# Kernel optimization log

Hardware: AMD Instinct MI355X
Metric: run time of the kernel (lower is better)

## Reference

```python
import jax, jax.numpy as jnp
import numpy as np

N_NODES = 100000
N_EDGES = 1600000
DIM = 128


def setup_inputs() -> dict:
    key = jax.random.key(0)
    k1, k2, k3, k4 = jax.random.split(key, 4)
    x = jax.random.normal(k1, (N_NODES, DIM), dtype=jnp.float32)
    edge_index = jax.random.randint(k2, (2, N_EDGES), 0, N_NODES, dtype=jnp.int64)
    scale = 1.0 / np.sqrt(DIM)
    W1 = jax.random.normal(k3, (DIM, DIM), dtype=jnp.float32) * scale
    W2 = jax.random.normal(k4, (DIM, DIM), dtype=jnp.float32) * scale
    b1 = jnp.zeros((DIM,), dtype=jnp.float32)
    b2 = jnp.zeros((DIM,), dtype=jnp.float32)
    return {"x": x, "edge_index": edge_index, "W1": W1, "b1": b1, "W2": W2, "b2": b2}


def _gcn_conv(x, src, dst, dinv, W, b, n):
    # linear transform first (PyG GCNConv), then normalized scatter-add aggregation
    h = x @ W                                   # [N, out]
    norm = dinv[src] * dinv[dst]                # [E+N]
    msg = h[src] * norm[:, None]                # [E+N, out]
    agg = jax.ops.segment_sum(msg, dst, num_segments=n)
    return agg + b


def reference(x, edge_index, W1, b1, W2, b2):
    n = x.shape[0]
    loops = jnp.arange(n, dtype=edge_index.dtype)
    src = jnp.concatenate([edge_index[0], loops])  # add self-loops
    dst = jnp.concatenate([edge_index[1], loops])
    deg = jax.ops.segment_sum(jnp.ones_like(src, dtype=x.dtype), dst, num_segments=n)
    dinv = jnp.where(deg > 0, jax.lax.rsqrt(deg), 0.0)  # D^{-1/2}
    h = _gcn_conv(x, src, dst, dinv, W1, b1, n)
    h = jax.nn.relu(h)
    out = _gcn_conv(h, src, dst, dinv, W2, b2, n)
    return out
```

## Files before the change

### kernel.cpp

```cpp
#include <hip/hip_runtime.h>
#include <hip/hip_bf16.h>
#include <hip/hip_fp16.h>

#define NN 100000
#define DIM 128
#define NB 391
#define BCAP 5120
#define GTILES ((NN + 63) / 64)
#define STP 130

typedef _Float16 f16x8 __attribute__((ext_vector_type(8)));
typedef float f32x4 __attribute__((ext_vector_type(4)));

__global__ void k_zero(int* __restrict__ p, int n) {
    int i = blockIdx.x * blockDim.x + threadIdx.x;
    if (i < n) p[i] = 0;
}

__global__ void k_binA(const int* __restrict__ src, const int* __restrict__ dst,
                       int* __restrict__ bcur, int* __restrict__ binbuf, int E) {
    __shared__ int hist[4][NB];
    const int t  = threadIdx.x;
    const int wv = t >> 6;
    for (int i = t; i < 4 * NB; i += 256) ((int*)hist)[i] = 0;
    __syncthreads();

    const int e0 = blockIdx.x * 4096;
    int mys[16], myd[16];
#pragma unroll
    for (int i = 0; i < 16; ++i) {
        const int e = e0 + i * 256 + t;
        int d = -1, s = 0;
        if (e < E) {
            d = dst[e];
            s = src[e];
            atomicAdd(&hist[wv][d >> 8], 1);
        }
        mys[i] = s;
        myd[i] = d;
    }
    __syncthreads();

    for (int b = t; b < NB; b += 256) {
        const int h0 = hist[0][b], h1 = hist[1][b], h2 = hist[2][b], h3 = hist[3][b];
        const int tot = h0 + h1 + h2 + h3;
        const int base = tot ? atomicAdd(&bcur[b], tot) : 0;
        hist[0][b] = base;
        hist[1][b] = base + h0;
        hist[2][b] = base + h0 + h1;
        hist[3][b] = base + h0 + h1 + h2;
    }
    __syncthreads();

#pragma unroll
    for (int i = 0; i < 16; ++i) {
        const int d = myd[i];
        if (d >= 0) {
            const int b = d >> 8;
            const int p = atomicAdd(&hist[wv][b], 1);
            if (p < BCAP) binbuf[b * BCAP + p] = mys[i] | ((d & 255) << 17);
        }
    }
}

__global__ void k_binCount(const int* __restrict__ bcur, const int* __restrict__ binbuf,
                           int* __restrict__ degi, float* __restrict__ dinv,
                           int* __restrict__ bsum) {
    __shared__ int cnt[4][256];
    __shared__ int red[256];
    const int b  = blockIdx.x;
    const int t  = threadIdx.x;
    const int wv = t >> 6;
#pragma unroll
    for (int w = 0; w < 4; ++w) cnt[w][t] = 0;
    __syncthreads();
    const int n = min(bcur[b], BCAP);
    const int* p = &binbuf[b * BCAP];
    for (int i = t; i < n; i += 256) atomicAdd(&cnt[wv][p[i] >> 17], 1);
    __syncthreads();
    const int node = b * 256 + t;
    const int c = cnt[0][t] + cnt[1][t] + cnt[2][t] + cnt[3][t];
    if (node < NN) {
        degi[node] = c;
        dinv[node] = rsqrtf((float)(c + 1));
    }
    red[t] = (node < NN) ? c : 0;
    __syncthreads();
    for (int d = 128; d > 0; d >>= 1) {
        if (t < d) red[t] += red[t + d];
        __syncthreads();
    }
    if (t == 0) bsum[b] = red[0];
}

__global__ void k_scan2(int* __restrict__ bsum, int nb) {
    __shared__ int s[1024];
    const int t = threadIdx.x;
    const int v = (t < nb) ? bsum[t] : 0;
    s[t] = v;
    __syncthreads();
    int acc = v;
    for (int d = 1; d < 1024; d <<= 1) {
        const int o = (t >= d) ? s[t - d] : 0;
        __syncthreads();
        acc += o;
        s[t] = acc;
        __syncthreads();
    }
    if (t < nb) bsum[t] = acc - v;
}

__global__ void k_gemm1(const float* __restrict__ inF, const float* __restrict__ W,
                        const float* __restrict__ dinv, _Float16* __restrict__ outH,
                        const int* __restrict__ degi, const int* __restrict__ bsum,
                        int* __restrict__ rowptr, const int* __restrict__ bcur,
                        const int* __restrict__ binbuf, int* __restrict__ csr) {
    __shared__ int s[256];
    __shared__ int cur[256];
    __shared__ _Float16 st[64][STP];
    const int t = threadIdx.x;

    if (blockIdx.x < NB) {
        const int b = blockIdx.x;
        const int node = b * 256 + t;
        const int deg = (node < NN) ? degi[node] : 0;
        s[t] = deg;
        __syncthreads();
        int acc = deg;
        for (int d = 1; d < 256; d <<= 1) {
            const int o = (t >= d) ? s[t - d] : 0;
            __syncthreads();
            acc += o;
            s[t] = acc;
            __syncthreads();
        }
        const int ex = acc - deg + bsum[b];
        cur[t] = ex;
        if (node < NN) {
            rowptr[node] = ex;
            if (node == NN - 1) rowptr[NN] = ex + deg;
        }
        __syncthreads();
        const int n = min(bcur[b], BCAP);
        const int* p = &binbuf[b * BCAP];
        for (int i = t; i < n; i += 256) {
            const int v = p[i];
            const int pos = atomicAdd(&cur[v >> 17], 1);
            csr[pos] = v & 0x1FFFF;
        }
        return;
    }

    const int tile = blockIdx.x - NB;
    const int row0 = tile * 64;
    const int wv   = t >> 6;
    const int l    = t & 63;
    const int l15  = l & 15;
    const int lk8  = (l >> 4) << 3;
    const int colw = wv << 5;

    f16x8 bf[2][4];
#pragma unroll
    for (int ct = 0; ct < 2; ++ct)
#pragma unroll
        for (int kt = 0; kt < 4; ++kt) {
            const int nn = colw + ct * 16 + l15;
            const int k0 = kt * 32 + lk8;
            f16x8 v;
#pragma unroll
            for (int j = 0; j < 8; ++j) v[j] = (_Float16)W[(k0 + j) * DIM + nn];
            bf[ct][kt] = v;
        }

    f32x4 acc[4][2];
#pragma unroll
    for (int rt = 0; rt < 4; ++rt)
#pragma unroll
        for (int ct = 0; ct < 2; ++ct) acc[rt][ct] = (f32x4){0.f, 0.f, 0.f, 0.f};

#pragma unroll
    for (int rt = 0; rt < 4; ++rt) {
        int row = row0 + rt * 16 + l15;
        row = min(row, NN - 1);
        f16x8 a[4];
#pragma unroll
        for (int kt = 0; kt < 4; ++kt) {
            const int k0 = kt * 32 + lk8;
            const float4 v0 = *(const float4*)&inF[row * DIM + k0];
            const float4 v1 = *(const float4*)&inF[row * DIM + k0 + 4];
            f16x8 v;
            v[0] = (_Float16)v0.x; v[1] = (_Float16)v0.y;
            v[2] = (_Float16)v0.z; v[3] = (_Float16)v0.w;
            v[4] = (_Float16)v1.x; v[5] = (_Float16)v1.y;
            v[6] = (_Float16)v1.z; v[7] = (_Float16)v1.w;
            a[kt] = v;
        }
#pragma unroll
        for (int ct = 0; ct < 2; ++ct)
#pragma unroll
            for (int kt = 0; kt < 4; ++kt)
                acc[rt][ct] = __builtin_amdgcn_mfma_f32_16x16x32_f16(a[kt], bf[ct][kt],
                                                                    acc[rt][ct], 0, 0, 0);
    }

#pragma unroll
    for (int rt = 0; rt < 4; ++rt)
#pragma unroll
        for (int r = 0; r < 4; ++r) {
            const int lr = rt * 16 + ((l >> 4) << 2) + r;
            const float d = dinv[min(row0 + lr, NN - 1)];
            st[lr][colw + l15]      = (_Float16)(acc[rt][0][r] * d);
            st[lr][colw + 16 + l15] = (_Float16)(acc[rt][1][r] * d);
        }
    __syncthreads();
#pragma unroll
    for (int i = 0; i < 4; ++i) {
        const int lr  = (wv << 4) + (i << 2) + (l >> 4);
        const int row = row0 + lr;
        if (row < NN) {
            const uint4 v = *(const uint4*)&st[lr][l15 << 3];
            *(uint4*)&outH[row * DIM + (l15 << 3)] = v;
        }
    }
}

__global__ void k_gemm2(const _Float16* __restrict__ inH, const float* __restrict__ W,
                        const float* __restrict__ dinv, _Float16* __restrict__ outH) {
    __shared__ _Float16 st[64][STP];
    const int t = threadIdx.x;
    const int row0 = blockIdx.x * 64;
    const int wv   = t >> 6;
    const int l    = t & 63;
    const int l15  = l & 15;
    const int lk8  = (l >> 4) << 3;
    const int colw = wv << 5;

    f16x8 bf[2][4];
#pragma unroll
    for (int ct = 0; ct < 2; ++ct)
#pragma unroll
        for (int kt = 0; kt < 4; ++kt) {
            const int nn = colw + ct * 16 + l15;
            const int k0 = kt * 32 + lk8;
            f16x8 v;
#pragma unroll
            for (int j = 0; j < 8; ++j) v[j] = (_Float16)W[(k0 + j) * DIM + nn];
            bf[ct][kt] = v;
        }

    f32x4 acc[4][2];
#pragma unroll
    for (int rt = 0; rt < 4; ++rt)
#pragma unroll
        for (int ct = 0; ct < 2; ++ct) acc[rt][ct] = (f32x4){0.f, 0.f, 0.f, 0.f};

#pragma unroll
    for (int rt = 0; rt < 4; ++rt) {
        int row = row0 + rt * 16 + l15;
        row = min(row, NN - 1);
        f16x8 a[4];
#pragma unroll
        for (int kt = 0; kt < 4; ++kt)
            a[kt] = *(const f16x8*)&inH[row * DIM + kt * 32 + lk8];
#pragma unroll
        for (int ct = 0; ct < 2; ++ct)
#pragma unroll
            for (int kt = 0; kt < 4; ++kt)
                acc[rt][ct] = __builtin_amdgcn_mfma_f32_16x16x32_f16(a[kt], bf[ct][kt],
                                                                    acc[rt][ct], 0, 0, 0);
    }

#pragma unroll
    for (int rt = 0; rt < 4; ++rt)
#pragma unroll
        for (int r = 0; r < 4; ++r) {
            const int lr = rt * 16 + ((l >> 4) << 2) + r;
            const float d = dinv[min(row0 + lr, NN - 1)];
            st[lr][colw + l15]      = (_Float16)(acc[rt][0][r] * d);
            st[lr][colw + 16 + l15] = (_Float16)(acc[rt][1][r] * d);
        }
    __syncthreads();
#pragma unroll
    for (int i = 0; i < 4; ++i) {
        const int lr  = (wv << 4) + (i << 2) + (l >> 4);
        const int row = row0 + lr;
        if (row < NN) {
            const uint4 v = *(const uint4*)&st[lr][l15 << 3];
            *(uint4*)&outH[row * DIM + (l15 << 3)] = v;
        }
    }
}

template <int FINAL>
__global__ void k_gather(const _Float16* __restrict__ hsp, _Float16* __restrict__ aggH,
                         float* __restrict__ outF, const int* __restrict__ csr,
                         const int* __restrict__ rowptr, const float* __restrict__ dinv,
                         const float* __restrict__ bias) {
    const __half* __restrict__ hs = (const __half*)hsp;
    const int w = (blockIdx.x * blockDim.x + threadIdx.x) >> 6;
    if (w >= NN) return;
    const int lane = threadIdx.x & 63;
    const int off  = lane << 1;

    const int start = __builtin_amdgcn_readfirstlane(rowptr[w]);
    const int end   = __builtin_amdgcn_readfirstlane(rowptr[w + 1]);

    float2 a0 = __half22float2(*(const __half2*)&hs[w * DIM + off]);
    float2 a1 = {0.f, 0.f}, a2 = {0.f, 0.f}, a3 = {0.f, 0.f};

    int j = start;
    for (; j + 3 < end; j += 4) {
        const int s0 = __builtin_amdgcn_readfirstlane(csr[j]);
        const int s1 = __builtin_amdgcn_readfirstlane(csr[j + 1]);
        const int s2 = __builtin_amdgcn_readfirstlane(csr[j + 2]);
        const int s3 = __builtin_amdgcn_readfirstlane(csr[j + 3]);
        const float2 v0 = __half22float2(*(const __half2*)&hs[s0 * DIM + off]);
        const float2 v1 = __half22float2(*(const __half2*)&hs[s1 * DIM + off]);
        const float2 v2 = __half22float2(*(const __half2*)&hs[s2 * DIM + off]);
        const float2 v3 = __half22float2(*(const __half2*)&hs[s3 * DIM + off]);
        a0.x += v0.x; a0.y += v0.y;
        a1.x += v1.x; a1.y += v1.y;
        a2.x += v2.x; a2.y += v2.y;
        a3.x += v3.x; a3.y += v3.y;
    }
    for (; j < end; ++j) {
        const int s0 = __builtin_amdgcn_readfirstlane(csr[j]);
        const float2 v0 = __half22float2(*(const __half2*)&hs[s0 * DIM + off]);
        a0.x += v0.x; a0.y += v0.y;
    }

    const float d = dinv[w];
    const float2 bb = {bias[off], bias[off + 1]};
    float2 r = {a0.x + a1.x + a2.x + a3.x, a0.y + a1.y + a2.y + a3.y};
    if constexpr (FINAL) {
        float2 o;
        o.x = fmaf(d, r.x, bb.x);
        o.y = fmaf(d, r.y, bb.y);
        *(float2*)&outF[w * DIM + off] = o;
    } else {
        r.x = fmaxf(fmaf(d, r.x, bb.x), 0.f);
        r.y = fmaxf(fmaf(d, r.y, bb.y), 0.f);
        *(__half2*)&aggH[w * DIM + off] = __floats2half2_rn(r.x, r.y);
    }
}

extern "C" void kernel_launch(void* const* d_in, const int* in_sizes, int n_in,
                              void* d_out, int out_size, void* d_ws, size_t ws_size,
                              hipStream_t stream) {
    const float* x  = (const float*)d_in[0];
    const int*   ei = (const int*)d_in[1];
    const float* W1 = (const float*)d_in[2];
    const float* b1 = (const float*)d_in[3];
    const float* W2 = (const float*)d_in[4];
    const float* b2 = (const float*)d_in[5];
    float* out = (float*)d_out;

    const int E = in_sizes[1] / 2;
    const int* src = ei;
    const int* dst = ei + E;

    char* ws = (char*)d_ws;
    float*    dinv   = (float*)(ws);
    int*      degi   = (int*)  (ws + (1  << 20));
    int*      rowptr = (int*)  (ws + (2  << 20));
    int*      bsum   = (int*)  (ws + (3  << 20));
    int*      bcur   = (int*)  (ws + (3  << 20) + 65536);
    int*      csr    = (int*)  (ws + (4  << 20));
    int*      binbuf = (int*)  (ws + (11 << 20));
    _Float16* hs     = (_Float16*)(ws + (20 << 20));
    _Float16* aggH   = (_Float16*)(ws + (47 << 20));
    _Float16* hs2    = (_Float16*)(ws + (74 << 20));

    const int ABLK = (E + 4095) / 4096;

    k_zero    <<<(NB + 255) / 256, 256, 0, stream>>>(bcur, NB);
    k_binA    <<<ABLK, 256, 0, stream>>>(src, dst, bcur, binbuf, E);
    k_binCount<<<NB, 256, 0, stream>>>(bcur, binbuf, degi, dinv, bsum);
    k_scan2   <<<1, 1024, 0, stream>>>(bsum, NB);

    k_gemm1<<<NB + GTILES, 256, 0, stream>>>(x, W1, dinv, hs, degi, bsum,
                                             rowptr, bcur, binbuf, csr);
    k_gather<0><<<(NN * 64) / 256, 256, 0, stream>>>(hs, aggH, nullptr, csr, rowptr,
                                                     dinv, b1);

    k_gemm2<<<GTILES, 256, 0, stream>>>(aggH, W2, dinv, hs2);
    k_gather<1><<<(NN * 64) / 256, 256, 0, stream>>>(hs2, nullptr, out, csr, rowptr,
                                                     dinv, b2);
}
```

Before: 225.7 us.

## Fold degree counting into CSR build, pre-transpose weights, move dinv scaling into gather

Removes the separate bin-count kernel. The block scan now runs directly on per-bin edge counts, and degree counting, dinv and rowptr are computed inside the CSR-building blocks of gemm1. Because dinv is no longer available when the GEMM tiles run, layer-1 source-side dinv scaling moves into gather1, which loads dinv per neighbour. W1 and W2 are pre-transposed to fp16 once so GEMM blocks can load B fragments as vectors, and the gather loops are unrolled to 8. The per-edge dinv loads in gather1 add extra scattered memory traffic in exchange for the removed launch and the overlap of CSR building with the GEMM.

```diff
diff --git a/kernel.cpp b/kernel.cpp
--- a/kernel.cpp
+++ b/kernel.cpp
@@ -12,9 +12,22 @@
 typedef _Float16 f16x8 __attribute__((ext_vector_type(8)));
 typedef float f32x4 __attribute__((ext_vector_type(4)));
 
-__global__ void k_zero(int* __restrict__ p, int n) {
-    int i = blockIdx.x * blockDim.x + threadIdx.x;
-    if (i < n) p[i] = 0;
+__global__ void k_init(const float* __restrict__ W1, const float* __restrict__ W2,
+                       int* __restrict__ bcur, _Float16* __restrict__ Wt1,
+                       _Float16* __restrict__ Wt2) {
+    const int b = blockIdx.x;
+    const int t = threadIdx.x;
+    if (b < 2) {
+        const int i = b * 256 + t;
+        if (i < NB) bcur[i] = 0;
+        return;
+    }
+    const int idx = (b - 2) * 256 + t;
+    const int which = idx >> 14;
+    const int i = idx & 16383;
+    const int n = i >> 7, k = i & 127;
+    if (which == 0) Wt1[n * DIM + k] = (_Float16)W1[k * DIM + n];
+    else            Wt2[n * DIM + k] = (_Float16)W2[k * DIM + n];
 }
 
 __global__ void k_binA(const int* __restrict__ src, const int* __restrict__ dst,
@@ -63,89 +76,70 @@
     }
 }
 
-__global__ void k_binCount(const int* __restrict__ bcur, const int* __restrict__ binbuf,
-                           int* __restrict__ degi, float* __restrict__ dinv,
-                           int* __restrict__ bsum) {
-    __shared__ int cnt[4][256];
-    __shared__ int red[256];
-    const int b  = blockIdx.x;
+__global__ void k_scan2(const int* __restrict__ bcur, int* __restrict__ bbase, int nb) {
+    __shared__ int s[512];
+    const int t = threadIdx.x;
+    const int v = (t < nb) ? bcur[t] : 0;
+    s[t] = v;
+    __syncthreads();
+    int acc = v;
+    for (int d = 1; d < 512; d <<= 1) {
+        const int o = (t >= d) ? s[t - d] : 0;
+        __syncthreads();
+        acc += o;
+        s[t] = acc;
+        __syncthreads();
+    }
+    if (t < nb) bbase[t] = acc - v;
+}
+
+__global__ void k_gemm1(const float* __restrict__ inF, const _Float16* __restrict__ Wt,
+                        _Float16* __restrict__ outH, const int* __restrict__ bbase,
+                        const int* __restrict__ bcur, const int* __restrict__ binbuf,
+                        int* __restrict__ rowptr, float* __restrict__ dinv,
+                        int* __restrict__ csr) {
+    __shared__ int cnt4[4][256];
+    __shared__ int sc[256];
+    __shared__ _Float16 st[64][STP];
     const int t  = threadIdx.x;
     const int wv = t >> 6;
-#pragma unroll
-    for (int w = 0; w < 4; ++w) cnt[w][t] = 0;
-    __syncthreads();
-    const int n = min(bcur[b], BCAP);
-    const int* p = &binbuf[b * BCAP];
-    for (int i = t; i < n; i += 256) atomicAdd(&cnt[wv][p[i] >> 17], 1);
-    __syncthreads();
-    const int node = b * 256 + t;
-    const int c = cnt[0][t] + cnt[1][t] + cnt[2][t] + cnt[3][t];
-    if (node < NN) {
-        degi[node] = c;
-        dinv[node] = rsqrtf((float)(c + 1));
-    }
-    red[t] = (node < NN) ? c : 0;
-    __syncthreads();
-    for (int d = 128; d > 0; d >>= 1) {
-        if (t < d) red[t] += red[t + d];
-        __syncthreads();
-    }
-    if (t == 0) bsum[b] = red[0];
-}
-
-__global__ void k_scan2(int* __restrict__ bsum, int nb) {
-    __shared__ int s[1024];
-    const int t = threadIdx.x;
-    const int v = (t < nb) ? bsum[t] : 0;
-    s[t] = v;
-    __syncthreads();
-    int acc = v;
-    for (int d = 1; d < 1024; d <<= 1) {
-        const int o = (t >= d) ? s[t - d] : 0;
-        __syncthreads();
-        acc += o;
-        s[t] = acc;
-        __syncthreads();
-    }
-    if (t < nb) bsum[t] = acc - v;
-}
-
-__global__ void k_gemm1(const float* __restrict__ inF, const float* __restrict__ W,
-                        const float* __restrict__ dinv, _Float16* __restrict__ outH,
-                        const int* __restrict__ degi, const int* __restrict__ bsum,
-                        int* __restrict__ rowptr, const int* __restrict__ bcur,
-                        const int* __restrict__ binbuf, int* __restrict__ csr) {
-    __shared__ int s[256];
-    __shared__ int cur[256];
-    __shared__ _Float16 st[64][STP];
-    const int t = threadIdx.x;
 
     if (blockIdx.x < NB) {
         const int b = blockIdx.x;
         const int node = b * 256 + t;
-        const int deg = (node < NN) ? degi[node] : 0;
-        s[t] = deg;
-        __syncthreads();
-        int acc = deg;
+#pragma unroll
+        for (int w = 0; w < 4; ++w) cnt4[w][t] = 0;
+        __syncthreads();
+        const int n_e = min(bcur[b], BCAP);
+        const int* p = &binbuf[b * BCAP];
+        for (int i = t; i < n_e; i += 256) atomicAdd(&cnt4[wv][p[i] >> 17], 1);
+        __syncthreads();
+        const int c0 = cnt4[0][t], c1 = cnt4[1][t], c2 = cnt4[2][t], c3 = cnt4[3][t];
+        const int c = c0 + c1 + c2 + c3;
+        if (node < NN) dinv[node] = rsqrtf((float)(c + 1));
+        sc[t] = c;
+        __syncthreads();
+        int acc = c;
         for (int d = 1; d < 256; d <<= 1) {
-            const int o = (t >= d) ? s[t - d] : 0;
+            const int o = (t >= d) ? sc[t - d] : 0;
             __syncthreads();
             acc += o;
-            s[t] = acc;
+            sc[t] = acc;
             __syncthreads();
         }
-        const int ex = acc - deg + bsum[b];
-        cur[t] = ex;
+        const int ex = acc - c + bbase[b];
         if (node < NN) {
             rowptr[node] = ex;
-            if (node == NN - 1) rowptr[NN] = ex + deg;
-        }
-        __syncthreads();
-        const int n = min(bcur[b], BCAP);
-        const int* p = &binbuf[b * BCAP];
-        for (int i = t; i < n; i += 256) {
+            if (node == NN - 1) rowptr[NN] = ex + c;
+        }
+        cnt4[0][t] = ex;
+        cnt4[1][t] = ex + c0;
+        cnt4[2][t] = ex + c0 + c1;
+        cnt4[3][t] = ex + c0 + c1 + c2;
+        __syncthreads();
+        for (int i = t; i < n_e; i += 256) {
             const int v = p[i];
-            const int pos = atomicAdd(&cur[v >> 17], 1);
+            const int pos = atomicAdd(&cnt4[wv][v >> 17], 1);
             csr[pos] = v & 0x1FFFF;
         }
         return;
@@ -153,7 +147,6 @@
 
     const int tile = blockIdx.x - NB;
     const int row0 = tile * 64;
-    const int wv   = t >> 6;
     const int l    = t & 63;
     const int l15  = l & 15;
     const int lk8  = (l >> 4) << 3;
@@ -163,14 +156,8 @@
 #pragma unroll
     for (int ct = 0; ct < 2; ++ct)
 #pragma unroll
-        for (int kt = 0; kt < 4; ++kt) {
-            const int nn = colw + ct * 16 + l15;
-            const int k0 = kt * 32 + lk8;
-            f16x8 v;
-#pragma unroll
-            for (int j = 0; j < 8; ++j) v[j] = (_Float16)W[(k0 + j) * DIM + nn];
-            bf[ct][kt] = v;
-        }
+        for (int kt = 0; kt < 4; ++kt)
+            bf[ct][kt] = *(const f16x8*)&Wt[(colw + ct * 16 + l15) * DIM + kt * 32 + lk8];
 
     f32x4 acc[4][2];
 #pragma unroll
@@ -208,9 +195,8 @@
 #pragma unroll
         for (int r = 0; r < 4; ++r) {
             const int lr = rt * 16 + ((l >> 4) << 2) + r;
-            const float d = dinv[min(row0 + lr, NN - 1)];
-            st[lr][colw + l15]      = (_Float16)(acc[rt][0][r] * d);
-            st[lr][colw + 16 + l15] = (_Float16)(acc[rt][1][r] * d);
+            st[lr][colw + l15]      = (_Float16)acc[rt][0][r];
+            st[lr][colw + 16 + l15] = (_Float16)acc[rt][1][r];
         }
     __syncthreads();
 #pragma unroll
@@ -224,7 +210,7 @@
     }
 }
 
-__global__ void k_gemm2(const _Float16* __restrict__ inH, const float* __restrict__ W,
+__global__ void k_gemm2(const _Float16* __restrict__ inH, const _Float16* __restrict__ Wt,
                         const float* __restrict__ dinv, _Float16* __restrict__ outH) {
     __shared__ _Float16 st[64][STP];
     const int t = threadIdx.x;
@@ -239,14 +225,8 @@
 #pragma unroll
     for (int ct = 0; ct < 2; ++ct)
 #pragma unroll
-        for (int kt = 0; kt < 4; ++kt) {
-            const int nn = colw + ct * 16 + l15;
-            const int k0 = kt * 32 + lk8;
-            f16x8 v;
-#pragma unroll
-            for (int j = 0; j < 8; ++j) v[j] = (_Float16)W[(k0 + j) * DIM + nn];
-            bf[ct][kt] = v;
-        }
+        for (int kt = 0; kt < 4; ++kt)
+            bf[ct][kt] = *(const f16x8*)&Wt[(colw + ct * 16 + l15) * DIM + kt * 32 + lk8];
 
     f32x4 acc[4][2];
 #pragma unroll
@@ -291,11 +271,9 @@
     }
 }
 
-template <int FINAL>
-__global__ void k_gather(const _Float16* __restrict__ hsp, _Float16* __restrict__ aggH,
-                         float* __restrict__ outF, const int* __restrict__ csr,
-                         const int* __restrict__ rowptr, const float* __restrict__ dinv,
-                         const float* __restrict__ bias) {
+__global__ void k_gather1(const _Float16* __restrict__ hsp, _Float16* __restrict__ aggH,
+                          const int* __restrict__ csr, const int* __restrict__ rowptr,
+                          const float* __restrict__ dinv, const float* __restrict__ bias) {
     const __half* __restrict__ hs = (const __half*)hsp;
     const int w = (blockIdx.x * blockDim.x + threadIdx.x) >> 6;
     if (w >= NN) return;
@@ -304,24 +282,98 @@
 
     const int start = __builtin_amdgcn_readfirstlane(rowptr[w]);
     const int end   = __builtin_amdgcn_readfirstlane(rowptr[w + 1]);
-
-    float2 a0 = __half22float2(*(const __half2*)&hs[w * DIM + off]);
-    float2 a1 = {0.f, 0.f}, a2 = {0.f, 0.f}, a3 = {0.f, 0.f};
+    const float dw  = dinv[w];
+
+    float2 a0 = {0.f, 0.f}, a1 = {0.f, 0.f}, a2 = {0.f, 0.f}, a3 = {0.f, 0.f};
+    {
+        const float2 v = __half22float2(*(const __half2*)&hs[w * DIM + off]);
+        a0.x = dw * v.x; a0.y = dw * v.y;
+    }
 
     int j = start;
-    for (; j + 3 < end; j += 4) {
+    for (; j + 7 < end; j += 8) {
         const int s0 = __builtin_amdgcn_readfirstlane(csr[j]);
         const int s1 = __builtin_amdgcn_readfirstlane(csr[j + 1]);
         const int s2 = __builtin_amdgcn_readfirstlane(csr[j + 2]);
         const int s3 = __builtin_amdgcn_readfirstlane(csr[j + 3]);
+        const int s4 = __builtin_amdgcn_readfirstlane(csr[j + 4]);
+        const int s5 = __builtin_amdgcn_readfirstlane(csr[j + 5]);
+        const int s6 = __builtin_amdgcn_readfirstlane(csr[j + 6]);
+        const int s7 = __builtin_amdgcn_readfirstlane(csr[j + 7]);
+        const float d0 = dinv[s0], d1 = dinv[s1], d2 = dinv[s2], d3 = dinv[s3];
+        const float d4 = dinv[s4], d5 = dinv[s5], d6 = dinv[s6], d7 = dinv[s7];
         const float2 v0 = __half22float2(*(const __half2*)&hs[s0 * DIM + off]);
         const float2 v1 = __half22float2(*(const __half2*)&hs[s1 * DIM + off]);
         const float2 v2 = __half22float2(*(const __half2*)&hs[s2 * DIM + off]);
         const float2 v3 = __half22float2(*(const __half2*)&hs[s3 * DIM + off]);
+        const float2 v4 = __half22float2(*(const __half2*)&hs[s4 * DIM + off]);
+        const float2 v5 = __half22float2(*(const __half2*)&hs[s5 * DIM + off]);
+        const float2 v6 = __half22float2(*(const __half2*)&hs[s6 * DIM + off]);
+        const float2 v7 = __half22float2(*(const __half2*)&hs[s7 * DIM + off]);
+        a0.x = fmaf(d0, v0.x, a0.x); a0.y = fmaf(d0, v0.y, a0.y);
+        a1.x = fmaf(d1, v1.x, a1.x); a1.y = fmaf(d1, v1.y, a1.y);
+        a2.x = fmaf(d2, v2.x, a2.x); a2.y = fmaf(d2, v2.y, a2.y);
+        a3.x = fmaf(d3, v3.x, a3.x); a3.y = fmaf(d3, v3.y, a3.y);
+        a0.x = fmaf(d4, v4.x, a0.x); a0.y = fmaf(d4, v4.y, a0.y);
+        a1.x = fmaf(d5, v5.x, a1.x); a1.y = fmaf(d5, v5.y, a1.y);
+        a2.x = fmaf(d6, v6.x, a2.x); a2.y = fmaf(d6, v6.y, a2.y);
+        a3.x = fmaf(d7, v7.x, a3.x); a3.y = fmaf(d7, v7.y, a3.y);
+    }
+    for (; j < end; ++j) {
+        const int s0 = __builtin_amdgcn_readfirstlane(csr[j]);
+        const float d0 = dinv[s0];
+        const float2 v0 = __half22float2(*(const __half2*)&hs[s0 * DIM + off]);
+        a0.x = fmaf(d0, v0.x, a0.x); a0.y = fmaf(d0, v0.y, a0.y);
+    }
+
+    const float2 bb = {bias[off], bias[off + 1]};
+    float2 r = {a0.x + a1.x + a2.x + a3.x, a0.y + a1.y + a2.y + a3.y};
+    r.x = fmaxf(fmaf(dw, r.x, bb.x), 0.f);
+    r.y = fmaxf(fmaf(dw, r.y, bb.y), 0.f);
+    *(__half2*)&aggH[w * DIM + off] = __floats2half2_rn(r.x, r.y);
+}
+
+__global__ void k_gather2(const _Float16* __restrict__ hsp, float* __restrict__ outF,
+                          const int* __restrict__ csr, const int* __restrict__ rowptr,
+                          const float* __restrict__ dinv, const float* __restrict__ bias) {
+    const __half* __restrict__ hs = (const __half*)hsp;
+    const int w = (blockIdx.x * blockDim.x + threadIdx.x) >> 6;
+    if (w >= NN) return;
+    const int lane = threadIdx.x & 63;
+    const int off  = lane << 1;
+
+    const int start = __builtin_amdgcn_readfirstlane(rowptr[w]);
+    const int end   = __builtin_amdgcn_readfirstlane(rowptr[w + 1]);
+
+    float2 a0 = __half22float2(*(const __half2*)&hs[w * DIM + off]);
+    float2 a1 = {0.f, 0.f}, a2 = {0.f, 0.f}, a3 = {0.f, 0.f};
+
+    int j = start;
+    for (; j + 7 < end; j += 8) {
+        const int s0 = __builtin_amdgcn_readfirstlane(csr[j]);
+        const int s1 = __builtin_amdgcn_readfirstlane(csr[j + 1]);
+        const int s2 = __builtin_amdgcn_readfirstlane(csr[j + 2]);
+        const int s3 = __builtin_amdgcn_readfirstlane(csr[j + 3]);
+        const int s4 = __builtin_amdgcn_readfirstlane(csr[j + 4]);
+        const int s5 = __builtin_amdgcn_readfirstlane(csr[j + 5]);
+        const int s6 = __builtin_amdgcn_readfirstlane(csr[j + 6]);
+        const int s7 = __builtin_amdgcn_readfirstlane(csr[j + 7]);
+        const float2 v0 = __half22float2(*(const __half2*)&hs[s0 * DIM + off]);
+        const float2 v1 = __half22float2(*(const __half2*)&hs[s1 * DIM + off]);
+        const float2 v2 = __half22float2(*(const __half2*)&hs[s2 * DIM + off]);
+        const float2 v3 = __half22float2(*(const __half2*)&hs[s3 * DIM + off]);
+        const float2 v4 = __half22float2(*(const __half2*)&hs[s4 * DIM + off]);
+        const float2 v5 = __half22float2(*(const __half2*)&hs[s5 * DIM + off]);
+        const float2 v6 = __half22float2(*(const __half2*)&hs[s6 * DIM + off]);
+        const float2 v7 = __half22float2(*(const __half2*)&hs[s7 * DIM + off]);
         a0.x += v0.x; a0.y += v0.y;
         a1.x += v1.x; a1.y += v1.y;
         a2.x += v2.x; a2.y += v2.y;
         a3.x += v3.x; a3.y += v3.y;
+        a0.x += v4.x; a0.y += v4.y;
+        a1.x += v5.x; a1.y += v5.y;
+        a2.x += v6.x; a2.y += v6.y;
+        a3.x += v7.x; a3.y += v7.y;
     }
     for (; j < end; ++j) {
         const int s0 = __builtin_amdgcn_readfirstlane(csr[j]);
@@ -332,16 +384,10 @@
     const float d = dinv[w];
     const float2 bb = {bias[off], bias[off + 1]};
     float2 r = {a0.x + a1.x + a2.x + a3.x, a0.y + a1.y + a2.y + a3.y};
-    if constexpr (FINAL) {
-        float2 o;
-        o.x = fmaf(d, r.x, bb.x);
-        o.y = fmaf(d, r.y, bb.y);
-        *(float2*)&outF[w * DIM + off] = o;
-    } else {
-        r.x = fmaxf(fmaf(d, r.x, bb.x), 0.f);
-        r.y = fmaxf(fmaf(d, r.y, bb.y), 0.f);
-        *(__half2*)&aggH[w * DIM + off] = __floats2half2_rn(r.x, r.y);
-    }
+    float2 o;
+    o.x = fmaf(d, r.x, bb.x);
+    o.y = fmaf(d, r.y, bb.y);
+    *(float2*)&outF[w * DIM + off] = o;
 }
 
 extern "C" void kernel_launch(void* const* d_in, const int* in_sizes, int n_in,
@@ -361,10 +407,11 @@
 
     char* ws = (char*)d_ws;
     float*    dinv   = (float*)(ws);
-    int*      degi   = (int*)  (ws + (1  << 20));
     int*      rowptr = (int*)  (ws + (2  << 20));
-    int*      bsum   = (int*)  (ws + (3  << 20));
+    int*      bbase  = (int*)  (ws + (3  << 20));
     int*      bcur   = (int*)  (ws + (3  << 20) + 65536);
+    _Float16* Wt1    = (_Float16*)(ws + (3 << 20) + 131072);
+    _Float16* Wt2    = (_Float16*)(ws + (3 << 20) + 196608);
     int*      csr    = (int*)  (ws + (4  << 20));
     int*      binbuf = (int*)  (ws + (11 << 20));
     _Float16* hs     = (_Float16*)(ws + (20 << 20));
@@ -373,17 +420,14 @@
 
     const int ABLK = (E + 4095) / 4096;
 
-    k_zero    <<<(NB + 255) / 256, 256, 0, stream>>>(bcur, NB);
-    k_binA    <<<ABLK, 256, 0, stream>>>(src, dst, bcur, binbuf, E);
-    k_binCount<<<NB, 256, 0, stream>>>(bcur, binbuf, degi, dinv, bsum);
-    k_scan2   <<<1, 1024, 0, stream>>>(bsum, NB);
-
-    k_gemm1<<<NB + GTILES, 256, 0, stream>>>(x, W1, dinv, hs, degi, bsum,
-                                             rowptr, bcur, binbuf, csr);
-    k_gather<0><<<(NN * 64) / 256, 256, 0, stream>>>(hs, aggH, nullptr, csr, rowptr,
-                                                     dinv, b1);
-
-    k_gemm2<<<GTILES, 256, 0, stream>>>(aggH, W2, dinv, hs2);
-    k_gather<1><<<(NN * 64) / 256, 256, 0, stream>>>(hs2, nullptr, out, csr, rowptr,
-                                                     dinv, b2);
-}
+    k_init <<<130, 256, 0, stream>>>(W1, W2, bcur, Wt1, Wt2);
+    k_binA <<<ABLK, 256, 0, stream>>>(src, dst, bcur, binbuf, E);
+    k_scan2<<<1, 512, 0, stream>>>(bcur, bbase, NB);
+
+    k_gemm1<<<NB + GTILES, 256, 0, stream>>>(x, Wt1, hs, bbase, bcur, binbuf,
+                                             rowptr, dinv, csr);
+    k_gather1<<<(NN * 64) / 256, 256, 0, stream>>>(hs, aggH, csr, rowptr, dinv, b1);
+
+    k_gemm2<<<GTILES, 256, 0, stream>>>(aggH, Wt2, dinv, hs2);
+    k_gather2<<<(NN * 64) / 256, 256, 0, stream>>>(hs2, out, csr, rowptr, dinv, b2);
+}
```

Measured after the change: 225.7 us. Within noise of the previous version (-0.0%).
